# Optimization experiments

Measured on AMD Instinct MI355X. Metric: run time of the kernel, lower is better.

Reference implementation:

```python
import jax, jax.numpy as jnp
import numpy as np

N, E, G = 50000, 800000, 64
IN_NODE, OUT_NODE, IN_EDGE = 16, 20, 16
HID_E, N_ACT, HID_C = 64, 8, 256
BN_EPS = 1e-5


def setup_inputs() -> dict:
    key = jax.random.key(0)
    ks = jax.random.split(key, 12)
    def w(i, shape, scale=0.05):
        return jax.random.normal(ks[i], shape, jnp.float32) * scale
    return {
        "x": jax.random.normal(ks[0], (N, IN_NODE), jnp.float32),
        "edge_attr": jax.random.normal(ks[1], (E, IN_EDGE), jnp.float32),
        "a": jax.random.normal(ks[2], (G, N_ACT), jnp.float32),
        "edge_index": jax.random.randint(ks[3], (2, E), 0, N),
        "batch": jnp.sort(jax.random.randint(ks[4], (N,), 0, G)),
        # edge-conditioning MLP: Lin(16,64) -> BN(64) -> ReLU -> Lin(64, 16*20)
        "W1": w(5, (IN_EDGE, HID_E)), "b1": jnp.zeros((HID_E,), jnp.float32),
        "gamma": jnp.ones((HID_E,), jnp.float32), "beta": jnp.zeros((HID_E,), jnp.float32),
        "W2": w(6, (HID_E, IN_NODE * OUT_NODE)), "b2": jnp.zeros((IN_NODE * OUT_NODE,), jnp.float32),
        # NNConv root weight + bias
        "root_w": w(7, (IN_NODE, OUT_NODE)), "bias": jnp.zeros((OUT_NODE,), jnp.float32),
        # critic head: Lin(20+8,256) -> ReLU -> Lin(256,1)
        "Wc1": w(8, (OUT_NODE + N_ACT, HID_C)), "bc1": jnp.zeros((HID_C,), jnp.float32),
        "Wc2": w(9, (HID_C, 1)), "bc2": jnp.zeros((1,), jnp.float32),
    }


def reference(x, edge_attr, a, W1, b1, gamma, beta, W2, b2, root_w, bias,
              Wc1, bc1, Wc2, bc2, edge_index, batch):
    # edge-conditioning MLP (BatchNorm in training mode: batch stats over edges)
    h = edge_attr @ W1 + b1                              # [E, 64]
    mu = jnp.mean(h, axis=0)
    var = jnp.mean(jnp.square(h - mu), axis=0)           # biased var, as BN fwd
    h = (h - mu) * jax.lax.rsqrt(var + BN_EPS) * gamma + beta
    h = jax.nn.relu(h)
    w_e = (h @ W2 + b2).reshape(E, IN_NODE, OUT_NODE)    # per-edge weight matrix

    src, dst = edge_index[0], edge_index[1]
    msg = jnp.einsum('ei,eio->eo', x[src], w_e)          # gather + per-edge matvec [E, 20]
    aggr = jax.ops.segment_sum(msg, dst, num_segments=N) # scatter-add (NNConv aggr='add')
    out = x @ root_w + aggr + bias                       # [N, 20]

    # global mean pool over graphs
    sums = jax.ops.segment_sum(out, batch, num_segments=G)            # [G, 20]
    cnt = jax.ops.segment_sum(jnp.ones((N, 1), out.dtype), batch, num_segments=G)
    pooled = sums / jnp.maximum(cnt, 1.0)

    z = jnp.concatenate([pooled, a], axis=1)             # [G, 28]
    z = jax.nn.relu(z @ Wc1 + bc1)
    return z @ Wc2 + bc2                                 # [G, 1]
```

## Files before the change

kernel.cpp:

```cpp
#include <hip/hip_runtime.h>


#define E_EDGES   800000
#define N_NODES   50000
#define G_GRAPHS  64
#define EDGE_GRID 3072
#define NGROUPS   50000
#define GSTRIDE   3072
#define NSUP      256
#define STAT_GRID 512
#define QSCALE    131072.0f
#define QINV      (1.0f / 131072.0f)

typedef _Float16 f16x2 __attribute__((ext_vector_type(2)));
typedef _Float16 f16x8 __attribute__((ext_vector_type(8)));
typedef __fp16   fp16x2 __attribute__((ext_vector_type(2)));
typedef float    f32x4 __attribute__((ext_vector_type(4)));
typedef unsigned u32x4 __attribute__((ext_vector_type(4)));

union H2U { f16x2 h; unsigned u; };
union F8U { f16x8 v; f16x2 h2[4]; u32x4 u4; };

__device__ __forceinline__ f16x2 pkrtz(float a, float b) {
  fp16x2 r = __builtin_amdgcn_cvt_pkrtz(a, b);
  return __builtin_bit_cast(f16x2, r);
}

__device__ __forceinline__ int q17(float x) {
  float r = __builtin_fmaf(x, QSCALE, 12582912.0f);
  return __builtin_bit_cast(int, r) - 0x4B400000;
}

__global__ __launch_bounds__(256) void setup_kernel(
    const float* __restrict__ W2, const float* __restrict__ b2,
    const float* __restrict__ W1, const float* __restrict__ x,
    const float* __restrict__ ea, unsigned* __restrict__ Bbuf,
    unsigned* __restrict__ Bw1, unsigned* __restrict__ xh,
    float* __restrict__ gstatsT)
{
  __shared__ float red[4][272];
  const int b = blockIdx.x, tid = threadIdx.x;
  if (b < STAT_GRID) {
    int lane = tid & 63, wave = tid >> 6;
    int nl = lane & 15, q = lane >> 4;
    int gw = b * 4 + wave;
    f32x4 acc = (f32x4){0.f, 0.f, 0.f, 0.f};
    float ms = 0.f;
    for (int c0 = gw; c0 < E_EDGES / 32; c0 += STAT_GRID * 4) {
      const float* p = ea + (size_t)(c0 * 32 + q * 8) * 16 + nl;
      float v0 = p[0],  v1 = p[16], v2 = p[32], v3 = p[48];
      float v4 = p[64], v5 = p[80], v6 = p[96], v7 = p[112];
      ms += (v0 + v1) + (v2 + v3) + (v4 + v5) + (v6 + v7);
      F8U av;
      av.h2[0] = pkrtz(v0, v1); av.h2[1] = pkrtz(v2, v3);
      av.h2[2] = pkrtz(v4, v5); av.h2[3] = pkrtz(v6, v7);
      acc = __builtin_amdgcn_mfma_f32_16x16x32_f16(av.v, av.v, acc, 0, 0, 0);
    }
    ms += __shfl_xor(ms, 16, 64);
    ms += __shfl_xor(ms, 32, 64);
#pragma unroll
    for (int r = 0; r < 4; ++r) red[wave][(q * 4 + r) * 16 + nl] = acc[r];
    if (q == 0) red[wave][256 + nl] = ms;
    __syncthreads();
    for (int v = tid; v < 272; v += 256)
      gstatsT[(size_t)v * STAT_GRID + b] =
          red[0][v] + red[1][v] + red[2][v] + red[3][v];
  } else if (b < STAT_GRID + 70) {
    int idx = (b - STAT_GRID) * 256 + tid;
    if (idx < 33 * 512) {
      int r = idx & 3, lane = (idx >> 2) & 63, nt = (idx >> 8) & 1,
          s = idx >> 9;
      int q = lane >> 4, nl = lane & 15, n = nt * 16 + nl;
      float v0 = 0.f, v1 = 0.f;
      if (n < 20) {
        if (s < 32) {
          int K0 = s * 32 + q * 8 + 2 * r;
          v0 = W2[(K0 >> 4) * 320 + (K0 & 15) * 20 + n];
          v1 = W2[((K0 + 1) >> 4) * 320 + ((K0 + 1) & 15) * 20 + n];
        } else if (q < 2) {
          int i0 = q * 8 + 2 * r;
          v0 = b2[i0 * 20 + n];
          v1 = b2[(i0 + 1) * 20 + n];
        }
      }
      H2U pk; pk.h = pkrtz(v0, v1);
      Bbuf[idx] = pk.u;
    } else {
      int idx2 = idx - 33 * 512;
      int r = idx2 & 3, lane = (idx2 >> 2) & 63, nt = idx2 >> 8;
      int q = lane >> 4, nl = lane & 15, n = nt * 16 + nl;
      int k0 = q * 8 + 2 * r;
      float v0 = (k0 < 16)     ? W1[k0 * 64 + n]       : 0.f;
      float v1 = (k0 + 1 < 16) ? W1[(k0 + 1) * 64 + n] : 0.f;
      H2U pk; pk.h = pkrtz(v0, v1);
      Bw1[idx2] = pk.u;
    }
  } else {
    int i = (b - STAT_GRID - 70) * 256 + tid;
    if (i < N_NODES * 8) {
      H2U pk; pk.h = pkrtz(x[2 * i], x[2 * i + 1]);
      xh[i] = pk.u;
    }
  }
}

__global__ __launch_bounds__(256) void mid_kernel(
    const float* __restrict__ gstatsT, const float* __restrict__ W1,
    const float* __restrict__ b1, const float* __restrict__ gamma,
    const float* __restrict__ beta, const float* __restrict__ x,
    const int* __restrict__ batch, float* __restrict__ sc,
    float* __restrict__ sh, float* __restrict__ sumx,
    float* __restrict__ cntf)
{
  const int t = threadIdx.x;
  if (blockIdx.x == G_GRAPHS) {
    __shared__ float S[272];
    for (int v = t; v < 272; v += 256) {
      const float* p = gstatsT + (size_t)v * STAT_GRID;
      float s0 = 0.f, s1 = 0.f, s2 = 0.f, s3 = 0.f;
      for (int bb = 0; bb < STAT_GRID; bb += 4) {
        s0 += p[bb]; s1 += p[bb + 1]; s2 += p[bb + 2]; s3 += p[bb + 3];
      }
      S[v] = (s0 + s1) + (s2 + s3);
    }
    __syncthreads();
    if (t < 64) {
      float w[16];
#pragma unroll
      for (int j = 0; j < 16; ++j) w[j] = W1[j * 64 + t];
      const float invE = 1.0f / (float)E_EDGES;
      float mw = 0.f;
#pragma unroll
      for (int j = 0; j < 16; ++j) mw += S[256 + j] * w[j];
      mw *= invE;
      float qf = 0.f;
      for (int j = 0; j < 16; ++j) {
        float tt = 0.f;
#pragma unroll
        for (int j2 = 0; j2 < 16; ++j2) tt += S[j * 16 + j2] * w[j2];
        qf += w[j] * tt;
      }
      qf *= invE;
      float b = b1[t];
      float meanH = mw + b;
      float eh2 = qf + 2.f * b * mw + b * b;
      float var = eh2 - meanH * meanH;
      float s = gamma[t] * rsqrtf(var + 1e-5f);
      sc[t] = s;
      sh[t] = beta[t] + (b - meanH) * s;
    }
  } else {
    int g = blockIdx.x;
    __shared__ int se[2];
    if (t < 2) {
      int key = g + t;
      int lo = 0, hi = N_NODES;
      while (lo < hi) {
        int mid = (lo + hi) >> 1;
        if (batch[mid] < key) lo = mid + 1; else hi = mid;
      }
      se[t] = lo;
    }
    __syncthreads();
    int start = se[0], end = se[1];
    int c = t & 15, rr = t >> 4;
    float s = 0.f;
    for (int n = start + rr; n < end; n += 16) s += x[(size_t)n * 16 + c];
    __shared__ float red[256];
    red[t] = s;
    __syncthreads();
#pragma unroll
    for (int st = 128; st >= 16; st >>= 1) {
      if (t < st) red[t] += red[t + st];
      __syncthreads();
    }
    if (t < 16) sumx[g * 16 + t] = red[t];
    if (t == 0) cntf[g] = (float)(end - start);
  }
}

__global__ __launch_bounds__(256, 3) void edge_kernel(
    const unsigned* __restrict__ xh, const float* __restrict__ ea,
    const int* __restrict__ ei, const int* __restrict__ batch,
    const float* __restrict__ sc, const float* __restrict__ sh,
    const unsigned* __restrict__ Bbuf, const unsigned* __restrict__ Bw1v,
    int* __restrict__ gpartI)
{
  __shared__ unsigned hh[4][640];
  __shared__ int gacc[1280];
  __shared__ float sEA[2][256];
  __shared__ unsigned sXH[2][128];
  __shared__ int sGE[2][16];
  __shared__ unsigned sBX[2][256];

  const int tid = threadIdx.x;
  const int w = tid >> 6;
  const int lane = tid & 63;
  const int nl = lane & 15, q = lane >> 4;
  const int qh = q & 1;
  const int kq = w;

  for (int v = tid; v < 1280; v += 256) gacc[v] = 0;

  F8U bb[8][2];
#pragma unroll
  for (int sl = 0; sl < 8; ++sl)
#pragma unroll
    for (int nt = 0; nt < 2; ++nt)
      bb[sl][nt].u4 =
          ((const u32x4*)Bbuf)[((kq * 8 + sl) * 2 + nt) * 64 + lane];
  F8U bw1; bw1.u4 = ((const u32x4*)Bw1v)[kq * 64 + lane];
  const float scv = sc[kq * 16 + nl];
  const float shv = sh[kq * 16 + nl];
  const int hrb = (q >> 1) * 20 + nl;

  if (w == 3) {
    u32x4 b0 = ((const u32x4*)Bbuf)[64 * 64 + lane];
    u32x4 b1 = ((const u32x4*)Bbuf)[65 * 64 + lane];
    *(u32x4*)&sBX[0][lane * 4] = b0;
    *(u32x4*)&sBX[1][lane * 4] = b1;
  }

  const int* srcp = ei;
  const int* dstp = ei + E_EDGES;
  int g = blockIdx.x;
  const int g1 = g + GSTRIDE;
  int srcg = 0, dstg = 0;

  {
    const int base0 = g * 16;
    f32x4 eA = (f32x4){0.f, 0.f, 0.f, 0.f}, eB = eA;
    if (q < 2) {
      const float* p = ea + (size_t)(base0 + nl) * 16 + q * 8;
      eA = *(const f32x4*)p;
      eB = *(const f32x4*)(p + 4);
    }
    F8U aEA;
    if (q < 2) {
      aEA.h2[0] = pkrtz(eA[0], eA[1]); aEA.h2[1] = pkrtz(eA[2], eA[3]);
      aEA.h2[2] = pkrtz(eB[0], eB[1]); aEA.h2[3] = pkrtz(eB[2], eB[3]);
    } else {
      aEA.u4 = (u32x4){0u, 0u, 0u, 0u};
    }
    f32x4 hD = __builtin_amdgcn_mfma_f32_16x16x32_f16(
        aEA.v, bw1.v, (f32x4){0.f, 0.f, 0.f, 0.f}, 0, 0, 0);
    u32x4 hwv;
#pragma unroll
    for (int r = 0; r < 4; ++r) {
      float h = fmaxf(hD[r] * scv + shv, 0.f);
      H2U pk; pk.h = pkrtz(h, h);
      hwv[r] = pk.u;
    }
    *(u32x4*)&hh[w][nl * 20 + q * 4] = hwv;

    if (w == 0) {
      if (lane < 32) {
        int s0 = srcp[base0 + (lane >> 1)];
        u32x4 xv = ((const u32x4*)xh)[s0 * 2 + (lane & 1)];
        *(u32x4*)&sXH[0][lane * 4] = xv;
        srcg = srcp[g1 * 16 + (lane >> 1)];
      }
    } else if (w == 2) {
      if (lane < 16) {
        int d0 = dstp[base0 + lane];
        sGE[0][lane] = batch[d0];
        dstg = dstp[g1 * 16 + lane];
      }
    } else if (w == 1) {
      f32x4 ev = *(const f32x4*)(ea + (size_t)g1 * 256 + lane * 4);
      *(f32x4*)&sEA[0][lane * 4] = ev;
    }
  }
  __syncthreads();

  int cur = 0;
  while (g < NGROUPS) {
    const int gn = g + GSTRIDE, g2 = gn + GSTRIDE;
    const bool hv = (gn < NGROUPS);

    u32x4 xstg;
    f32x4 estg;
    int gestg = 0, src2 = 0, dst2 = 0;
    if (w == 0) {
      if (lane < 32) {
        if (hv) xstg = ((const u32x4*)xh)[srcg * 2 + (lane & 1)];
        if (g2 < NGROUPS) src2 = srcp[g2 * 16 + (lane >> 1)];
      }
    } else if (w == 2) {
      if (lane < 16) {
        if (hv) gestg = batch[dstg];
        if (g2 < NGROUPS) dst2 = dstp[g2 * 16 + lane];
      }
    } else if (w == 1) {
      if (g2 < NGROUPS)
        estg = *(const f32x4*)(ea + (size_t)g2 * 256 + lane * 4);
    }

    F8U xcur;
    xcur.u4 = *(const u32x4*)&sXH[cur][(nl * 2 + qh) * 4];
    const int ge0 = sGE[cur][q * 4 + 0] * 20;
    const int ge1 = sGE[cur][q * 4 + 1] * 20;
    const int ge2v = sGE[cur][q * 4 + 2] * 20;
    const int ge3 = sGE[cur][q * 4 + 3] * 20;
    unsigned hu[8];
#pragma unroll
    for (int sl = 0; sl < 8; ++sl) hu[sl] = hh[w][cur * 320 + hrb + sl * 40];

    f32x4 hDn = (f32x4){0.f, 0.f, 0.f, 0.f};
    if (hv) {
      F8U aEA;
      if (q < 2) {
        f32x4 eA = *(const f32x4*)&sEA[cur][nl * 16 + q * 8];
        f32x4 eB = *(const f32x4*)&sEA[cur][nl * 16 + q * 8 + 4];
        aEA.h2[0] = pkrtz(eA[0], eA[1]); aEA.h2[1] = pkrtz(eA[2], eA[3]);
        aEA.h2[2] = pkrtz(eB[0], eB[1]); aEA.h2[3] = pkrtz(eB[2], eB[3]);
      } else {
        aEA.u4 = (u32x4){0u, 0u, 0u, 0u};
      }
      hDn = __builtin_amdgcn_mfma_f32_16x16x32_f16(
          aEA.v, bw1.v, (f32x4){0.f, 0.f, 0.f, 0.f}, 0, 0, 0);
    }

    f32x4 a00 = (f32x4){0.f, 0.f, 0.f, 0.f};
    f32x4 a01 = a00, a10 = a00, a11 = a00;
#pragma unroll
    for (int sl = 0; sl < 8; sl += 2) {
      H2U u0; u0.u = hu[sl];
      H2U u1; u1.u = hu[sl + 1];
      F8U av0, av1;
      av0.h2[0] = u0.h * xcur.h2[0];
      av0.h2[1] = u0.h * xcur.h2[1];
      av0.h2[2] = u0.h * xcur.h2[2];
      av0.h2[3] = u0.h * xcur.h2[3];
      av1.h2[0] = u1.h * xcur.h2[0];
      av1.h2[1] = u1.h * xcur.h2[1];
      av1.h2[2] = u1.h * xcur.h2[2];
      av1.h2[3] = u1.h * xcur.h2[3];
      a00 = __builtin_amdgcn_mfma_f32_16x16x32_f16(av0.v, bb[sl][0].v, a00,
                                                   0, 0, 0);
      a10 = __builtin_amdgcn_mfma_f32_16x16x32_f16(av0.v, bb[sl][1].v, a10,
                                                   0, 0, 0);
      a01 = __builtin_amdgcn_mfma_f32_16x16x32_f16(av1.v, bb[sl + 1][0].v,
                                                   a01, 0, 0, 0);
      a11 = __builtin_amdgcn_mfma_f32_16x16x32_f16(av1.v, bb[sl + 1][1].v,
                                                   a11, 0, 0, 0);
    }
    if (kq == 3) {
      F8U bxa, bxb;
      bxa.u4 = *(const u32x4*)&sBX[0][lane * 4];
      bxb.u4 = *(const u32x4*)&sBX[1][lane * 4];
      F8U av;
      if (q < 2) av = xcur;
      else       av.u4 = (u32x4){0u, 0u, 0u, 0u};
      a00 = __builtin_amdgcn_mfma_f32_16x16x32_f16(av.v, bxa.v, a00,
                                                   0, 0, 0);
      a10 = __builtin_amdgcn_mfma_f32_16x16x32_f16(av.v, bxb.v, a10,
                                                   0, 0, 0);
    }
    const f32x4 acc0 = a00 + a01;
    const f32x4 acc1 = a10 + a11;

    if (hv) {
      u32x4 hwv;
#pragma unroll
      for (int r = 0; r < 4; ++r) {
        float h = fmaxf(hDn[r] * scv + shv, 0.f);
        H2U pk; pk.h = pkrtz(h, h);
        hwv[r] = pk.u;
      }
      *(u32x4*)&hh[w][(cur ^ 1) * 320 + nl * 20 + q * 4] = hwv;
    }
    if (w == 0) {
      if (lane < 32 && hv) *(u32x4*)&sXH[cur ^ 1][lane * 4] = xstg;
    } else if (w == 2) {
      if (lane < 16 && hv) sGE[cur ^ 1][lane] = gestg;
    } else if (w == 1) {
      if (g2 < NGROUPS) *(f32x4*)&sEA[cur ^ 1][lane * 4] = estg;
    }

    {
      atomicAdd(&gacc[ge0 + nl], q17(acc0[0]));
      if (nl < 4) atomicAdd(&gacc[ge0 + 16 + nl], q17(acc1[0]));
      atomicAdd(&gacc[ge1 + nl], q17(acc0[1]));
      if (nl < 4) atomicAdd(&gacc[ge1 + 16 + nl], q17(acc1[1]));
      atomicAdd(&gacc[ge2v + nl], q17(acc0[2]));
      if (nl < 4) atomicAdd(&gacc[ge2v + 16 + nl], q17(acc1[2]));
      atomicAdd(&gacc[ge3 + nl], q17(acc0[3]));
      if (nl < 4) atomicAdd(&gacc[ge3 + 16 + nl], q17(acc1[3]));
    }

    __syncthreads();
    g = gn; cur ^= 1;
    srcg = src2; dstg = dst2;
  }

  const int ssup = blockIdx.x & (NSUP - 1);
  for (int v = tid; v < 1280; v += 256) {
    int gg = v / 20, o = v - gg * 20;
    atomicAdd(&gpartI[(gg * NSUP + ssup) * 20 + o], gacc[v]);
  }
}

__global__ __launch_bounds__(256) void critic_kernel(
    const int* __restrict__ gpartI, const float* __restrict__ sumx,
    const float* __restrict__ cntf, const float* __restrict__ root_w,
    const float* __restrict__ bias, const float* __restrict__ a,
    const float* __restrict__ Wc1, const float* __restrict__ bc1,
    const float* __restrict__ Wc2, const float* __restrict__ bc2,
    float* __restrict__ out)
{
  int g = blockIdx.x, t = threadIdx.x;
  __shared__ int part[240];
  __shared__ float pooled[20];
  if (t < 240) {
    int col = t % 20, r = t / 20;
    int s = 0;
    const int* gp = gpartI + (size_t)g * NSUP * 20;
    for (int sl = r; sl < NSUP; sl += 12) s += gp[sl * 20 + col];
    part[t] = s;
  }
  __syncthreads();
  if (t < 20) {
    int si = 0;
#pragma unroll
    for (int r = 0; r < 12; ++r) si += part[r * 20 + t];
    float s = (float)si * QINV;
    float cnt = cntf[g];
    float base = bias[t] * cnt;
#pragma unroll
    for (int i = 0; i < 16; ++i) base += sumx[g * 16 + i] * root_w[i * 20 + t];
    pooled[t] = (s + base) / fmaxf(cnt, 1.f);
  }
  __syncthreads();
  float z = bc1[t];
#pragma unroll
  for (int j = 0; j < 20; ++j) z += pooled[j] * Wc1[j * 256 + t];
#pragma unroll
  for (int j = 0; j < 8; ++j) z += a[g * 8 + j] * Wc1[(20 + j) * 256 + t];
  z = fmaxf(z, 0.f);
  float pr = z * Wc2[t];
#pragma unroll
  for (int off = 32; off >= 1; off >>= 1) pr += __shfl_down(pr, off, 64);
  __shared__ float red[4];
  if ((t & 63) == 0) red[t >> 6] = pr;
  __syncthreads();
  if (t == 0) out[g] = red[0] + red[1] + red[2] + red[3] + bc2[0];
}

extern "C" void kernel_launch(void* const* d_in, const int* in_sizes, int n_in,
                              void* d_out, int out_size, void* d_ws,
                              size_t ws_size, hipStream_t stream) {
  const float* x         = (const float*)d_in[0];
  const float* edge_attr = (const float*)d_in[1];
  const float* a         = (const float*)d_in[2];
  const int*   ei        = (const int*)d_in[3];
  const int*   batch     = (const int*)d_in[4];
  const float* W1        = (const float*)d_in[5];
  const float* b1        = (const float*)d_in[6];
  const float* gamma     = (const float*)d_in[7];
  const float* beta      = (const float*)d_in[8];
  const float* W2        = (const float*)d_in[9];
  const float* b2        = (const float*)d_in[10];
  const float* root_w    = (const float*)d_in[11];
  const float* bias      = (const float*)d_in[12];
  const float* Wc1       = (const float*)d_in[13];
  const float* bc1       = (const float*)d_in[14];
  const float* Wc2       = (const float*)d_in[15];
  const float* bc2       = (const float*)d_in[16];
  float* out = (float*)d_out;

  float* wsf     = (float*)d_ws;
  float* sc      = wsf;
  float* sh      = wsf + 64;
  float* sumx    = wsf + 128;
  float* cntf    = wsf + 1152;
  unsigned* Bw1  = (unsigned*)(wsf + 1216);
  unsigned* Bbuf = (unsigned*)(wsf + 2240);
  float* gstatsT = wsf + 19136;
  unsigned* xhp  = (unsigned*)(wsf + 158400);
  int* gpartI    = (int*)(wsf + 558400);

  (void)hipMemsetAsync(gpartI, 0, (size_t)G_GRAPHS * NSUP * 20 * sizeof(int),
                       stream);

  const int XCONV_BLOCKS = (N_NODES * 8 + 255) / 256;
  setup_kernel<<<STAT_GRID + 70 + XCONV_BLOCKS, 256, 0, stream>>>(
      W2, b2, W1, x, edge_attr, Bbuf, Bw1, xhp, gstatsT);
  mid_kernel<<<G_GRAPHS + 1, 256, 0, stream>>>(gstatsT, W1, b1, gamma, beta,
                                               x, batch, sc, sh, sumx, cntf);
  edge_kernel<<<EDGE_GRID, 256, 0, stream>>>(xhp, edge_attr, ei, batch, sc,
                                             sh, Bbuf, Bw1, gpartI);
  critic_kernel<<<G_GRAPHS, 256, 0, stream>>>(gpartI, sumx, cntf, root_w,
                                              bias, a, Wc1, bc1, Wc2, bc2,
                                              out);
}
```

Baseline: 237.2 us.

## Fuse BN stats finalize and per-graph x sums into setup kernel via last-block pattern

Removes the separate mid_kernel launch. Per-block BN statistics are now accumulated with float atomics into a global buffer, and a last-block counter lets the final stats block compute the BN scale and shift. The per-graph x-sum blocks move into the setup grid, and one memset now zeroes the stats, the counter and the partial buffer together. This saves a kernel launch and the serial reduction over 512 partials. In exchange it adds atomic contention and makes the stats sum order nondeterministic.

```diff
diff --git a/kernel.cpp b/kernel.cpp
--- a/kernel.cpp
+++ b/kernel.cpp
@@ -33,12 +33,18 @@
 
 __global__ __launch_bounds__(256) void setup_kernel(
     const float* __restrict__ W2, const float* __restrict__ b2,
-    const float* __restrict__ W1, const float* __restrict__ x,
-    const float* __restrict__ ea, unsigned* __restrict__ Bbuf,
-    unsigned* __restrict__ Bw1, unsigned* __restrict__ xh,
-    float* __restrict__ gstatsT)
+    const float* __restrict__ W1, const float* __restrict__ b1,
+    const float* __restrict__ gamma, const float* __restrict__ beta,
+    const float* __restrict__ x, const float* __restrict__ ea,
+    const int* __restrict__ batch,
+    unsigned* __restrict__ Bbuf, unsigned* __restrict__ Bw1,
+    unsigned* __restrict__ xh, float* __restrict__ sc,
+    float* __restrict__ sh, float* __restrict__ sumx,
+    float* __restrict__ cntf, float* __restrict__ statsG,
+    unsigned* __restrict__ ctr)
 {
   __shared__ float red[4][272];
+  __shared__ int lastB;
   const int b = blockIdx.x, tid = threadIdx.x;
   if (b < STAT_GRID) {
     int lane = tid & 63, wave = tid >> 6;
@@ -63,8 +69,45 @@
     if (q == 0) red[wave][256 + nl] = ms;
     __syncthreads();
     for (int v = tid; v < 272; v += 256)
-      gstatsT[(size_t)v * STAT_GRID + b] =
-          red[0][v] + red[1][v] + red[2][v] + red[3][v];
+      atomicAdd(&statsG[v],
+                (red[0][v] + red[1][v]) + (red[2][v] + red[3][v]));
+    __threadfence();
+    __syncthreads();
+    if (tid == 0) lastB = (atomicAdd(ctr, 1u) == STAT_GRID - 1);
+    __syncthreads();
+    if (lastB) {
+      __threadfence();
+      float* S = red[0];
+      for (int v = tid; v < 272; v += 256)
+        S[v] = atomicAdd(&statsG[v], 0.0f);
+      __syncthreads();
+      if (tid < 64) {
+        const int t = tid;
+        float w[16];
+#pragma unroll
+        for (int j = 0; j < 16; ++j) w[j] = W1[j * 64 + t];
+        const float invE = 1.0f / (float)E_EDGES;
+        float mw = 0.f;
+#pragma unroll
+        for (int j = 0; j < 16; ++j) mw += S[256 + j] * w[j];
+        mw *= invE;
+        float qf = 0.f;
+        for (int j = 0; j < 16; ++j) {
+          float tt = 0.f;
+#pragma unroll
+          for (int j2 = 0; j2 < 16; ++j2) tt += S[j * 16 + j2] * w[j2];
+          qf += w[j] * tt;
+        }
+        qf *= invE;
+        float bb = b1[t];
+        float meanH = mw + bb;
+        float eh2 = qf + 2.f * bb * mw + bb * bb;
+        float var = eh2 - meanH * meanH;
+        float s = gamma[t] * rsqrtf(var + 1e-5f);
+        sc[t] = s;
+        sh[t] = beta[t] + (bb - meanH) * s;
+      }
+    }
   } else if (b < STAT_GRID + 70) {
     int idx = (b - STAT_GRID) * 256 + tid;
     if (idx < 33 * 512) {
@@ -95,63 +138,11 @@
       H2U pk; pk.h = pkrtz(v0, v1);
       Bw1[idx2] = pk.u;
     }
-  } else {
-    int i = (b - STAT_GRID - 70) * 256 + tid;
-    if (i < N_NODES * 8) {
-      H2U pk; pk.h = pkrtz(x[2 * i], x[2 * i + 1]);
-      xh[i] = pk.u;
-    }
-  }
-}
-
-__global__ __launch_bounds__(256) void mid_kernel(
-    const float* __restrict__ gstatsT, const float* __restrict__ W1,
-    const float* __restrict__ b1, const float* __restrict__ gamma,
-    const float* __restrict__ beta, const float* __restrict__ x,
-    const int* __restrict__ batch, float* __restrict__ sc,
-    float* __restrict__ sh, float* __restrict__ sumx,
-    float* __restrict__ cntf)
-{
-  const int t = threadIdx.x;
-  if (blockIdx.x == G_GRAPHS) {
-    __shared__ float S[272];
-    for (int v = t; v < 272; v += 256) {
-      const float* p = gstatsT + (size_t)v * STAT_GRID;
-      float s0 = 0.f, s1 = 0.f, s2 = 0.f, s3 = 0.f;
-      for (int bb = 0; bb < STAT_GRID; bb += 4) {
-        s0 += p[bb]; s1 += p[bb + 1]; s2 += p[bb + 2]; s3 += p[bb + 3];
-      }
-      S[v] = (s0 + s1) + (s2 + s3);
-    }
-    __syncthreads();
-    if (t < 64) {
-      float w[16];
-#pragma unroll
-      for (int j = 0; j < 16; ++j) w[j] = W1[j * 64 + t];
-      const float invE = 1.0f / (float)E_EDGES;
-      float mw = 0.f;
-#pragma unroll
-      for (int j = 0; j < 16; ++j) mw += S[256 + j] * w[j];
-      mw *= invE;
-      float qf = 0.f;
-      for (int j = 0; j < 16; ++j) {
-        float tt = 0.f;
-#pragma unroll
-        for (int j2 = 0; j2 < 16; ++j2) tt += S[j * 16 + j2] * w[j2];
-        qf += w[j] * tt;
-      }
-      qf *= invE;
-      float b = b1[t];
-      float meanH = mw + b;
-      float eh2 = qf + 2.f * b * mw + b * b;
-      float var = eh2 - meanH * meanH;
-      float s = gamma[t] * rsqrtf(var + 1e-5f);
-      sc[t] = s;
-      sh[t] = beta[t] + (b - meanH) * s;
-    }
-  } else {
-    int g = blockIdx.x;
+  } else if (b < STAT_GRID + 70 + G_GRAPHS) {
+    int g = b - (STAT_GRID + 70);
     __shared__ int se[2];
+    __shared__ float redx[256];
+    const int t = tid;
     if (t < 2) {
       int key = g + t;
       int lo = 0, hi = N_NODES;
@@ -166,16 +157,21 @@
     int c = t & 15, rr = t >> 4;
     float s = 0.f;
     for (int n = start + rr; n < end; n += 16) s += x[(size_t)n * 16 + c];
-    __shared__ float red[256];
-    red[t] = s;
+    redx[t] = s;
     __syncthreads();
 #pragma unroll
     for (int st = 128; st >= 16; st >>= 1) {
-      if (t < st) red[t] += red[t + st];
+      if (t < st) redx[t] += redx[t + st];
       __syncthreads();
     }
-    if (t < 16) sumx[g * 16 + t] = red[t];
+    if (t < 16) sumx[g * 16 + t] = redx[t];
     if (t == 0) cntf[g] = (float)(end - start);
+  } else {
+    int i = (b - (STAT_GRID + 70 + G_GRAPHS)) * 256 + tid;
+    if (i < N_NODES * 8) {
+      H2U pk; pk.h = pkrtz(x[2 * i], x[2 * i + 1]);
+      xh[i] = pk.u;
+    }
   }
 }
 
@@ -476,18 +472,17 @@
   float* cntf    = wsf + 1152;
   unsigned* Bw1  = (unsigned*)(wsf + 1216);
   unsigned* Bbuf = (unsigned*)(wsf + 2240);
-  float* gstatsT = wsf + 19136;
-  unsigned* xhp  = (unsigned*)(wsf + 158400);
-  int* gpartI    = (int*)(wsf + 558400);
-
-  (void)hipMemsetAsync(gpartI, 0, (size_t)G_GRAPHS * NSUP * 20 * sizeof(int),
-                       stream);
+  unsigned* xhp  = (unsigned*)(wsf + 19136);
+  float* statsG  = wsf + 419136;
+  unsigned* ctr  = (unsigned*)(wsf + 419408);
+  int* gpartI    = (int*)(wsf + 419416);
+
+  (void)hipMemsetAsync(statsG, 0, (size_t)(272 + 8 + 327680) * 4, stream);
 
   const int XCONV_BLOCKS = (N_NODES * 8 + 255) / 256;
-  setup_kernel<<<STAT_GRID + 70 + XCONV_BLOCKS, 256, 0, stream>>>(
-      W2, b2, W1, x, edge_attr, Bbuf, Bw1, xhp, gstatsT);
-  mid_kernel<<<G_GRAPHS + 1, 256, 0, stream>>>(gstatsT, W1, b1, gamma, beta,
-                                               x, batch, sc, sh, sumx, cntf);
+  setup_kernel<<<STAT_GRID + 70 + G_GRAPHS + XCONV_BLOCKS, 256, 0, stream>>>(
+      W2, b2, W1, b1, gamma, beta, x, edge_attr, batch, Bbuf, Bw1, xhp,
+      sc, sh, sumx, cntf, statsG, ctr);
   edge_kernel<<<EDGE_GRID, 256, 0, stream>>>(xhp, edge_attr, ei, batch, sc,
                                              sh, Bbuf, Bw1, gpartI);
   critic_kernel<<<G_GRAPHS, 256, 0, stream>>>(gpartI, sumx, cntf, root_w,
```

New measurement: 273.0 us. +15.1%, slower.

## Use float LDS atomics, prepack edge attrs to fp16, prescale graph ids

Applied to the files above, without the earlier changes.

The per-graph accumulation moves from fixed-point integer LDS atomics (q17 quantization) to native float atomics in LDS and in the global partial buffer, which drops the quantize and dequantize arithmetic. Edge attributes are converted to packed fp16 when staged into shared memory, so the MFMA operand becomes a single 128-bit LDS load instead of two float4 loads plus conversions. Graph ids are stored premultiplied by 20 and read back as one int4. Float atomics make the summation order nondeterministic, and on some hardware LDS float atomics may be slower than integer ones.

```diff
diff --git a/kernel.cpp b/kernel.cpp
--- a/kernel.cpp
+++ b/kernel.cpp
@@ -9,8 +9,6 @@
 #define GSTRIDE   3072
 #define NSUP      256
 #define STAT_GRID 512
-#define QSCALE    131072.0f
-#define QINV      (1.0f / 131072.0f)
 
 typedef _Float16 f16x2 __attribute__((ext_vector_type(2)));
 typedef _Float16 f16x8 __attribute__((ext_vector_type(8)));
@@ -24,11 +22,6 @@
 __device__ __forceinline__ f16x2 pkrtz(float a, float b) {
   fp16x2 r = __builtin_amdgcn_cvt_pkrtz(a, b);
   return __builtin_bit_cast(f16x2, r);
-}
-
-__device__ __forceinline__ int q17(float x) {
-  float r = __builtin_fmaf(x, QSCALE, 12582912.0f);
-  return __builtin_bit_cast(int, r) - 0x4B400000;
 }
 
 __global__ __launch_bounds__(256) void setup_kernel(
@@ -184,11 +177,11 @@
     const int* __restrict__ ei, const int* __restrict__ batch,
     const float* __restrict__ sc, const float* __restrict__ sh,
     const unsigned* __restrict__ Bbuf, const unsigned* __restrict__ Bw1v,
-    int* __restrict__ gpartI)
+    float* __restrict__ gpartF)
 {
   __shared__ unsigned hh[4][640];
-  __shared__ int gacc[1280];
-  __shared__ float sEA[2][256];
+  __shared__ float gacc[1280];
+  __shared__ unsigned sEAh[2][128];
   __shared__ unsigned sXH[2][128];
   __shared__ int sGE[2][16];
   __shared__ unsigned sBX[2][256];
@@ -200,7 +193,7 @@
   const int qh = q & 1;
   const int kq = w;
 
-  for (int v = tid; v < 1280; v += 256) gacc[v] = 0;
+  for (int v = tid; v < 1280; v += 256) gacc[v] = 0.f;
 
   F8U bb[8][2];
 #pragma unroll
@@ -263,12 +256,15 @@
     } else if (w == 2) {
       if (lane < 16) {
         int d0 = dstp[base0 + lane];
-        sGE[0][lane] = batch[d0];
+        sGE[0][lane] = batch[d0] * 20;
         dstg = dstp[g1 * 16 + lane];
       }
     } else if (w == 1) {
       f32x4 ev = *(const f32x4*)(ea + (size_t)g1 * 256 + lane * 4);
-      *(f32x4*)&sEA[0][lane * 4] = ev;
+      H2U p0; p0.h = pkrtz(ev[0], ev[1]);
+      H2U p1; p1.h = pkrtz(ev[2], ev[3]);
+      sEAh[0][lane * 2]     = p0.u;
+      sEAh[0][lane * 2 + 1] = p1.u;
     }
   }
   __syncthreads();
@@ -288,7 +284,7 @@
       }
     } else if (w == 2) {
       if (lane < 16) {
-        if (hv) gestg = batch[dstg];
+        if (hv) gestg = batch[dstg] * 20;
         if (g2 < NGROUPS) dst2 = dstp[g2 * 16 + lane];
       }
     } else if (w == 1) {
@@ -298,10 +294,7 @@
 
     F8U xcur;
     xcur.u4 = *(const u32x4*)&sXH[cur][(nl * 2 + qh) * 4];
-    const int ge0 = sGE[cur][q * 4 + 0] * 20;
-    const int ge1 = sGE[cur][q * 4 + 1] * 20;
-    const int ge2v = sGE[cur][q * 4 + 2] * 20;
-    const int ge3 = sGE[cur][q * 4 + 3] * 20;
+    const int4 gev = *(const int4*)&sGE[cur][q * 4];
     unsigned hu[8];
 #pragma unroll
     for (int sl = 0; sl < 8; ++sl) hu[sl] = hh[w][cur * 320 + hrb + sl * 40];
@@ -310,10 +303,7 @@
     if (hv) {
       F8U aEA;
       if (q < 2) {
-        f32x4 eA = *(const f32x4*)&sEA[cur][nl * 16 + q * 8];
-        f32x4 eB = *(const f32x4*)&sEA[cur][nl * 16 + q * 8 + 4];
-        aEA.h2[0] = pkrtz(eA[0], eA[1]); aEA.h2[1] = pkrtz(eA[2], eA[3]);
-        aEA.h2[2] = pkrtz(eB[0], eB[1]); aEA.h2[3] = pkrtz(eB[2], eB[3]);
+        aEA.u4 = *(const u32x4*)&sEAh[cur][nl * 8 + q * 4];
       } else {
         aEA.u4 = (u32x4){0u, 0u, 0u, 0u};
       }
@@ -375,18 +365,23 @@
     } else if (w == 2) {
       if (lane < 16 && hv) sGE[cur ^ 1][lane] = gestg;
     } else if (w == 1) {
-      if (g2 < NGROUPS) *(f32x4*)&sEA[cur ^ 1][lane * 4] = estg;
+      if (g2 < NGROUPS) {
+        H2U p0; p0.h = pkrtz(estg[0], estg[1]);
+        H2U p1; p1.h = pkrtz(estg[2], estg[3]);
+        sEAh[cur ^ 1][lane * 2]     = p0.u;
+        sEAh[cur ^ 1][lane * 2 + 1] = p1.u;
+      }
     }
 
     {
-      atomicAdd(&gacc[ge0 + nl], q17(acc0[0]));
-      if (nl < 4) atomicAdd(&gacc[ge0 + 16 + nl], q17(acc1[0]));
-      atomicAdd(&gacc[ge1 + nl], q17(acc0[1]));
-      if (nl < 4) atomicAdd(&gacc[ge1 + 16 + nl], q17(acc1[1]));
-      atomicAdd(&gacc[ge2v + nl], q17(acc0[2]));
-      if (nl < 4) atomicAdd(&gacc[ge2v + 16 + nl], q17(acc1[2]));
-      atomicAdd(&gacc[ge3 + nl], q17(acc0[3]));
-      if (nl < 4) atomicAdd(&gacc[ge3 + 16 + nl], q17(acc1[3]));
+      atomicAdd(&gacc[gev.x + nl], acc0[0]);
+      if (nl < 4) atomicAdd(&gacc[gev.x + 16 + nl], acc1[0]);
+      atomicAdd(&gacc[gev.y + nl], acc0[1]);
+      if (nl < 4) atomicAdd(&gacc[gev.y + 16 + nl], acc1[1]);
+      atomicAdd(&gacc[gev.z + nl], acc0[2]);
+      if (nl < 4) atomicAdd(&gacc[gev.z + 16 + nl], acc1[2]);
+      atomicAdd(&gacc[gev.w + nl], acc0[3]);
+      if (nl < 4) atomicAdd(&gacc[gev.w + 16 + nl], acc1[3]);
     }
 
     __syncthreads();
@@ -397,12 +392,12 @@
   const int ssup = blockIdx.x & (NSUP - 1);
   for (int v = tid; v < 1280; v += 256) {
     int gg = v / 20, o = v - gg * 20;
-    atomicAdd(&gpartI[(gg * NSUP + ssup) * 20 + o], gacc[v]);
+    atomicAdd(&gpartF[(gg * NSUP + ssup) * 20 + o], gacc[v]);
   }
 }
 
 __global__ __launch_bounds__(256) void critic_kernel(
-    const int* __restrict__ gpartI, const float* __restrict__ sumx,
+    const float* __restrict__ gpartF, const float* __restrict__ sumx,
     const float* __restrict__ cntf, const float* __restrict__ root_w,
     const float* __restrict__ bias, const float* __restrict__ a,
     const float* __restrict__ Wc1, const float* __restrict__ bc1,
@@ -410,21 +405,20 @@
     float* __restrict__ out)
 {
   int g = blockIdx.x, t = threadIdx.x;
-  __shared__ int part[240];
+  __shared__ float part[240];
   __shared__ float pooled[20];
   if (t < 240) {
     int col = t % 20, r = t / 20;
-    int s = 0;
-    const int* gp = gpartI + (size_t)g * NSUP * 20;
+    float s = 0.f;
+    const float* gp = gpartF + (size_t)g * NSUP * 20;
     for (int sl = r; sl < NSUP; sl += 12) s += gp[sl * 20 + col];
     part[t] = s;
   }
   __syncthreads();
   if (t < 20) {
-    int si = 0;
-#pragma unroll
-    for (int r = 0; r < 12; ++r) si += part[r * 20 + t];
-    float s = (float)si * QINV;
+    float s = 0.f;
+#pragma unroll
+    for (int r = 0; r < 12; ++r) s += part[r * 20 + t];
     float cnt = cntf[g];
     float base = bias[t] * cnt;
 #pragma unroll
@@ -478,9 +472,9 @@
   unsigned* Bbuf = (unsigned*)(wsf + 2240);
   float* gstatsT = wsf + 19136;
   unsigned* xhp  = (unsigned*)(wsf + 158400);
-  int* gpartI    = (int*)(wsf + 558400);
-
-  (void)hipMemsetAsync(gpartI, 0, (size_t)G_GRAPHS * NSUP * 20 * sizeof(int),
+  float* gpartF  = wsf + 558400;
+
+  (void)hipMemsetAsync(gpartF, 0, (size_t)G_GRAPHS * NSUP * 20 * sizeof(float),
                        stream);
 
   const int XCONV_BLOCKS = (N_NODES * 8 + 255) / 256;
@@ -489,8 +483,8 @@
   mid_kernel<<<G_GRAPHS + 1, 256, 0, stream>>>(gstatsT, W1, b1, gamma, beta,
                                                x, batch, sc, sh, sumx, cntf);
   edge_kernel<<<EDGE_GRID, 256, 0, stream>>>(xhp, edge_attr, ei, batch, sc,
-                                             sh, Bbuf, Bw1, gpartI);
-  critic_kernel<<<G_GRAPHS, 256, 0, stream>>>(gpartI, sumx, cntf, root_w,
+                                             sh, Bbuf, Bw1, gpartF);
+  critic_kernel<<<G_GRAPHS, 256, 0, stream>>>(gpartF, sumx, cntf, root_w,
                                               bias, a, Wc1, bc1, Wc2, bc2,
                                               out);
 }
```

Result: slower. 499.3 us (+110.4%).
